# Optimization experiments

Hardware: AMD Instinct MI355X
Metric: run time of the kernel (lower is better)

The kernel has to match this reference:

```python
import jax, jax.numpy as jnp
import numpy as np

NUM_SEGMENTS = 64
HIDDEN = 1024
RANK = 16
N = 8192


def _xavier(key, shape):
    fan_in, fan_out = shape[-2], shape[-1]
    limit = (6.0 / (fan_in + fan_out)) ** 0.5
    return jax.random.uniform(key, shape, jnp.float32, -limit, limit)


def setup_inputs() -> dict:
    key = jax.random.key(0)
    k1, k2, k3, k4 = jax.random.split(key, 4)
    return {
        "math_hidden_states": jax.random.normal(k1, (N, HIDDEN), jnp.float32),
        "segment_ids": jax.random.randint(k2, (N,), 0, NUM_SEGMENTS, jnp.int64),
        "A_matrices": _xavier(k3, (NUM_SEGMENTS, HIDDEN, RANK)),
        "B_matrices": _xavier(k4, (NUM_SEGMENTS, RANK, HIDDEN)),
        "bias": jnp.zeros((NUM_SEGMENTS, HIDDEN), jnp.float32),
    }


def reference(math_hidden_states, segment_ids, A_matrices, B_matrices, bias):
    # gather per-token low-rank factors: A [N,H,R], B [N,R,H]
    gathered_A = A_matrices[segment_ids]
    gathered_B = B_matrices[segment_ids]
    # intermediate = B @ x  -> [N, R]
    intermediate = jnp.einsum('nrh,nh->nr', gathered_B, math_hidden_states)
    # transformed = A @ intermediate -> [N, H]
    transformed = jnp.einsum('nhr,nr->nh', gathered_A, intermediate)
    return transformed + bias[segment_ids]
```

## Files before the change

kernel.cpp:

```cpp
#include <hip/hip_runtime.h>

#define HID 1024
#define RANK 16
#define NSEG 64
#define G 16
#define NXCD 8


__global__ __launch_bounds__(1024) void k_hist_scan(
    const int* __restrict__ seg, int N,
    int* __restrict__ base_g, int* __restrict__ cursor_g,
    int* __restrict__ desc_g, int gtiles)
{
    __shared__ int hist[NSEG];
    __shared__ int ltot;
    const int tid = threadIdx.x;
    if (tid < NSEG) hist[tid] = 0;
    __syncthreads();
    for (int i = tid; i < N; i += 1024) atomicAdd(&hist[seg[i]], 1);
    __syncthreads();

    if (tid < 64) {
        const int h = hist[tid];
        const int p = (h + 15) & ~15;
        int v = p;
        #pragma unroll
        for (int off = 1; off < 64; off <<= 1) {
            int u = __shfl_up(v, off, 64);
            if (tid >= off) v += u;
        }
        const int b = v - p;
        base_g[tid]   = b;
        cursor_g[tid] = 0;
        if (tid == 63) ltot = v;
        const int nt = (h + 15) >> 4;
        for (int k = 0; k < nt; ++k) {
            const int cnt = min(16, h - (k << 4));
            desc_g[(b >> 4) + k] = (tid << 19) | (cnt << 14) | (b + (k << 4));
        }
    }
    __syncthreads();
    const int totTiles = ltot >> 4;
    for (int t = totTiles + tid; t < gtiles; t += 1024) desc_g[t] = -1;
}

__global__ __launch_bounds__(256) void k_scatter(
    const int* __restrict__ seg, int N,
    const int* __restrict__ base_g, int* __restrict__ cursor_g,
    int* __restrict__ sorted)
{
    const int i = blockIdx.x * 256 + threadIdx.x;
    if (i < N) {
        const int s = seg[i];
        const int pos = atomicAdd(&cursor_g[s], 1);
        sorted[base_g[s] + pos] = i;
    }
}

__global__ __launch_bounds__(256) void k_apply(
    const float* __restrict__ x,
    const int*   __restrict__ sorted,
    const int*   __restrict__ desc,
    const float* __restrict__ A,
    const float* __restrict__ B,
    const float* __restrict__ bias,
    float*       __restrict__ out,
    int chunkPerXcd)
{
    const int work = (blockIdx.x & (NXCD - 1)) * chunkPerXcd + (blockIdx.x >> 3);
    const int d = desc[work];
    if (d < 0) return;
    const int s     = d >> 19;
    const int cnt   = (d >> 14) & 31;
    const int start = d & 16383;

    const int tid  = threadIdx.x;
    const int lane = tid & 63;
    const int w    = tid >> 6;

    __shared__ float4 x_lds[G][HID / 4];
    __shared__ float  red[4][16][68];
    __shared__ float  inter_lds[G][RANK];

    const int n0 = sorted[start];

    #pragma unroll
    for (int jj = 0; jj < 4; ++jj) {
        const int j  = w * 4 + jj;
        const int nj = (j < cnt) ? sorted[start + j] : n0;
        const float4* xr = (const float4*)(x + (size_t)nj * HID);
        #pragma unroll
        for (int k = 0; k < 4; ++k)
            x_lds[j][k * 64 + lane] = xr[k * 64 + lane];
    }

    int n[G];
    #pragma unroll
    for (int j = 0; j < G; ++j)
        n[j] = (j < cnt) ? sorted[start + j] : n0;

    __syncthreads();

    const float4* B4 = (const float4*)(B + (size_t)s * RANK * HID);
    float acc[4][G];
    #pragma unroll
    for (int rr = 0; rr < 4; ++rr)
        #pragma unroll
        for (int j = 0; j < G; ++j) acc[rr][j] = 0.f;

    #pragma unroll
    for (int k = 0; k < 4; ++k) {
        float4 b[4];
        #pragma unroll
        for (int rr = 0; rr < 4; ++rr)
            b[rr] = B4[(size_t)(w * 4 + rr) * (HID / 4) + k * 64 + lane];
        #pragma unroll
        for (int j = 0; j < G; ++j) {
            const float4 xj = x_lds[j][k * 64 + lane];
            #pragma unroll
            for (int rr = 0; rr < 4; ++rr)
                acc[rr][j] += b[rr].x * xj.x + b[rr].y * xj.y
                            + b[rr].z * xj.z + b[rr].w * xj.w;
        }
    }

    const int v = lane & 15;
    const int q = lane >> 4;
    #pragma unroll
    for (int p = 0; p < 4; ++p) {
        #pragma unroll
        for (int idx = 0; idx < 16; ++idx)
            red[w][idx][lane] = acc[idx >> 2][p * 4 + (idx & 3)];
        const float4* rp = (const float4*)&red[w][v][q * 16];
        float4 r0 = rp[0], r1 = rp[1], r2 = rp[2], r3 = rp[3];
        float sum = ((r0.x + r0.y) + (r0.z + r0.w))
                  + ((r1.x + r1.y) + (r1.z + r1.w))
                  + ((r2.x + r2.y) + (r2.z + r2.w))
                  + ((r3.x + r3.y) + (r3.z + r3.w));
        sum += __shfl_xor(sum, 16, 64);
        sum += __shfl_xor(sum, 32, 64);
        if (lane < 16)
            inter_lds[p * 4 + (v & 3)][w * 4 + (v >> 2)] = sum;
    }
    __syncthreads();

    const float4* A4 = (const float4*)(A + (size_t)s * HID * RANK);
    float4 av[4][4];
    #pragma unroll
    for (int jh = 0; jh < 4; ++jh)
        #pragma unroll
        for (int qq = 0; qq < 4; ++qq)
            av[jh][qq] = A4[(size_t)(tid * 4 + jh) * (RANK / 4) + qq];
    const float4 bia = ((const float4*)(bias + (size_t)s * HID))[tid];

    #pragma unroll
    for (int j = 0; j < G; ++j) {
        const float4* I4 = (const float4*)inter_lds[j];
        float4 iv[4];
        #pragma unroll
        for (int qq = 0; qq < 4; ++qq) iv[qq] = I4[qq];
        float4 o = bia;
        float* op = (float*)&o;
        #pragma unroll
        for (int jh = 0; jh < 4; ++jh) {
            float a = 0.f;
            #pragma unroll
            for (int qq = 0; qq < 4; ++qq)
                a += av[jh][qq].x * iv[qq].x + av[jh][qq].y * iv[qq].y
                   + av[jh][qq].z * iv[qq].z + av[jh][qq].w * iv[qq].w;
            op[jh] += a;
        }
        if (j < cnt)
            ((float4*)(out + (size_t)n[j] * HID))[tid] = o;
    }
}

extern "C" void kernel_launch(void* const* d_in, const int* in_sizes, int n_in,
                              void* d_out, int out_size, void* d_ws, size_t ws_size,
                              hipStream_t stream) {
    const float* x    = (const float*)d_in[0];
    const int*   seg  = (const int*)d_in[1];
    const float* A    = (const float*)d_in[2];
    const float* B    = (const float*)d_in[3];
    const float* bias = (const float*)d_in[4];
    float* out = (float*)d_out;

    const int N = in_sizes[1];
    const int gtiles = (((N + G - 1) / G) + NSEG + 7) & ~7;

    int* wsi    = (int*)d_ws;
    int* base_g = wsi;
    int* cursor = wsi + NSEG;
    int* desc   = wsi + 2 * NSEG;
    int* sorted = wsi + 2 * NSEG + gtiles;

    k_hist_scan<<<1, 1024, 0, stream>>>(seg, N, base_g, cursor, desc, gtiles);
    k_scatter  <<<(N + 255) / 256, 256, 0, stream>>>(seg, N, base_g, cursor, sorted);
    k_apply    <<<gtiles, 256, 0, stream>>>(x, sorted, desc, A, B, bias, out,
                                            gtiles / NXCD);
}
```

Measured before the change: 143.0 us.

## Split fused low-rank apply into split-K intermediate and output kernels

The single fused gather/B-projection/A-projection kernel is replaced by two kernels. Tiles grow to 32 tokens per segment. The first kernel splits the hidden dimension into 4 chunks, keeps the B slice in registers, and writes partial rank-16 intermediates to workspace. The second kernel reduces the 4 partials and computes a 256-wide slice of the output per block. This targets more parallelism and no LDS staging of x, at the cost of an extra launch, a global round trip for the partials, and more padding per segment.

```diff
diff --git a/kernel.cpp b/kernel.cpp
--- a/kernel.cpp
+++ b/kernel.cpp
@@ -3,7 +3,8 @@
 #define HID 1024
 #define RANK 16
 #define NSEG 64
-#define G 16
+#define T 32
+#define KC 4
 #define NXCD 8
 
 
@@ -22,7 +23,7 @@
 
     if (tid < 64) {
         const int h = hist[tid];
-        const int p = (h + 15) & ~15;
+        const int p = (h + T - 1) & ~(T - 1);
         int v = p;
         #pragma unroll
         for (int off = 1; off < 64; off <<= 1) {
@@ -33,15 +34,14 @@
         base_g[tid]   = b;
         cursor_g[tid] = 0;
         if (tid == 63) ltot = v;
-        const int nt = (h + 15) >> 4;
+        const int nt = (h + T - 1) >> 5;
         for (int k = 0; k < nt; ++k) {
-            const int cnt = min(16, h - (k << 4));
-            desc_g[(b >> 4) + k] = (tid << 19) | (cnt << 14) | (b + (k << 4));
+            const int cnt = min(T, h - (k << 5));
+            desc_g[(b >> 5) + k] = (tid << 20) | (cnt << 14) | (b + (k << 5));
         }
     }
     __syncthreads();
-    const int totTiles = ltot >> 4;
-    for (int t = totTiles + tid; t < gtiles; t += 1024) desc_g[t] = -1;
+    for (int t = (ltot >> 5) + tid; t < gtiles; t += 1024) desc_g[t] = -1;
 }
 
 __global__ __launch_bounds__(256) void k_scatter(
@@ -57,80 +57,54 @@
     }
 }
 
-__global__ __launch_bounds__(256) void k_apply(
+__global__ __launch_bounds__(256) void k_inter(
     const float* __restrict__ x,
     const int*   __restrict__ sorted,
     const int*   __restrict__ desc,
-    const float* __restrict__ A,
     const float* __restrict__ B,
-    const float* __restrict__ bias,
-    float*       __restrict__ out,
+    float*       __restrict__ part,
     int chunkPerXcd)
 {
-    const int work = (blockIdx.x & (NXCD - 1)) * chunkPerXcd + (blockIdx.x >> 3);
-    const int d = desc[work];
+    const int bid  = blockIdx.x;
+    const int work = (bid & (NXCD - 1)) * chunkPerXcd + (bid >> 3);
+    const int tile = work >> 2;
+    const int c    = work & 3;
+    const int d = desc[tile];
     if (d < 0) return;
-    const int s     = d >> 19;
-    const int cnt   = (d >> 14) & 31;
+    const int s     = d >> 20;
+    const int cnt   = (d >> 14) & 63;
     const int start = d & 16383;
 
     const int tid  = threadIdx.x;
     const int lane = tid & 63;
     const int w    = tid >> 6;
 
-    __shared__ float4 x_lds[G][HID / 4];
-    __shared__ float  red[4][16][68];
-    __shared__ float  inter_lds[G][RANK];
+    __shared__ float red[4][16][68];
+
+    const float4* B4 = (const float4*)B + (size_t)s * (RANK * HID / 4);
+    float4 br[16];
+    #pragma unroll
+    for (int r = 0; r < 16; ++r)
+        br[r] = B4[r * (HID / 4) + c * 64 + lane];
 
     const int n0 = sorted[start];
+    const int v  = lane & 15;
+    const int q  = lane >> 4;
+    float* outp = part + ((size_t)tile * KC + c) * (T * RANK);
 
     #pragma unroll
-    for (int jj = 0; jj < 4; ++jj) {
-        const int j  = w * 4 + jj;
-        const int nj = (j < cnt) ? sorted[start + j] : n0;
-        const float4* xr = (const float4*)(x + (size_t)nj * HID);
+    for (int j = 0; j < 8; ++j) {
+        const int tok = w * 8 + j;
+        const int nj  = (tok < cnt) ? sorted[start + tok] : n0;
+        const float4 xv = ((const float4*)x)[(size_t)nj * (HID / 4) + c * 64 + lane];
+
+        float acc[16];
         #pragma unroll
-        for (int k = 0; k < 4; ++k)
-            x_lds[j][k * 64 + lane] = xr[k * 64 + lane];
-    }
-
-    int n[G];
-    #pragma unroll
-    for (int j = 0; j < G; ++j)
-        n[j] = (j < cnt) ? sorted[start + j] : n0;
-
-    __syncthreads();
-
-    const float4* B4 = (const float4*)(B + (size_t)s * RANK * HID);
-    float acc[4][G];
-    #pragma unroll
-    for (int rr = 0; rr < 4; ++rr)
+        for (int r = 0; r < 16; ++r)
+            acc[r] = br[r].x * xv.x + br[r].y * xv.y + br[r].z * xv.z + br[r].w * xv.w;
+
         #pragma unroll
-        for (int j = 0; j < G; ++j) acc[rr][j] = 0.f;
-
-    #pragma unroll
-    for (int k = 0; k < 4; ++k) {
-        float4 b[4];
-        #pragma unroll
-        for (int rr = 0; rr < 4; ++rr)
-            b[rr] = B4[(size_t)(w * 4 + rr) * (HID / 4) + k * 64 + lane];
-        #pragma unroll
-        for (int j = 0; j < G; ++j) {
-            const float4 xj = x_lds[j][k * 64 + lane];
-            #pragma unroll
-            for (int rr = 0; rr < 4; ++rr)
-                acc[rr][j] += b[rr].x * xj.x + b[rr].y * xj.y
-                            + b[rr].z * xj.z + b[rr].w * xj.w;
-        }
-    }
-
-    const int v = lane & 15;
-    const int q = lane >> 4;
-    #pragma unroll
-    for (int p = 0; p < 4; ++p) {
-        #pragma unroll
-        for (int idx = 0; idx < 16; ++idx)
-            red[w][idx][lane] = acc[idx >> 2][p * 4 + (idx & 3)];
+        for (int r = 0; r < 16; ++r) red[w][r][lane] = acc[r];
         const float4* rp = (const float4*)&red[w][v][q * 16];
         float4 r0 = rp[0], r1 = rp[1], r2 = rp[2], r3 = rp[3];
         float sum = ((r0.x + r0.y) + (r0.z + r0.w))
@@ -139,39 +113,65 @@
                   + ((r3.x + r3.y) + (r3.z + r3.w));
         sum += __shfl_xor(sum, 16, 64);
         sum += __shfl_xor(sum, 32, 64);
-        if (lane < 16)
-            inter_lds[p * 4 + (v & 3)][w * 4 + (v >> 2)] = sum;
-    }
-    __syncthreads();
-
-    const float4* A4 = (const float4*)(A + (size_t)s * HID * RANK);
-    float4 av[4][4];
+        if (lane < 16) outp[tok * RANK + v] = sum;
+    }
+}
+
+__global__ __launch_bounds__(256) void k_out(
+    const int*   __restrict__ sorted,
+    const int*   __restrict__ desc,
+    const float* __restrict__ A,
+    const float* __restrict__ bias,
+    const float* __restrict__ part,
+    float*       __restrict__ out,
+    int chunkPerXcd)
+{
+    const int bid  = blockIdx.x;
+    const int work = (bid & (NXCD - 1)) * chunkPerXcd + (bid >> 3);
+    const int tile = work >> 2;
+    const int hc   = work & 3;
+    const int d = desc[tile];
+    if (d < 0) return;
+    const int s     = d >> 20;
+    const int cnt   = (d >> 14) & 63;
+    const int start = d & 16383;
+
+    const int tid = threadIdx.x;
+
+    __shared__ float2 inter2[T * RANK / 2];
+    __shared__ int    tok_lds[T];
+
+    if (tid < T) tok_lds[tid] = (tid < cnt) ? sorted[start + tid] : -1;
+
+    {
+        const float2* p2 = (const float2*)(part + (size_t)tile * KC * (T * RANK));
+        float2 a0 = p2[tid], a1 = p2[256 + tid], a2 = p2[512 + tid], a3 = p2[768 + tid];
+        inter2[tid] = make_float2(a0.x + a1.x + a2.x + a3.x,
+                                  a0.y + a1.y + a2.y + a3.y);
+    }
+
+    const float4* A4 = (const float4*)A + (size_t)s * (HID * RANK / 4);
+    float4 av[4];
     #pragma unroll
-    for (int jh = 0; jh < 4; ++jh)
-        #pragma unroll
-        for (int qq = 0; qq < 4; ++qq)
-            av[jh][qq] = A4[(size_t)(tid * 4 + jh) * (RANK / 4) + qq];
-    const float4 bia = ((const float4*)(bias + (size_t)s * HID))[tid];
-
-    #pragma unroll
-    for (int j = 0; j < G; ++j) {
-        const float4* I4 = (const float4*)inter_lds[j];
-        float4 iv[4];
-        #pragma unroll
-        for (int qq = 0; qq < 4; ++qq) iv[qq] = I4[qq];
-        float4 o = bia;
-        float* op = (float*)&o;
-        #pragma unroll
-        for (int jh = 0; jh < 4; ++jh) {
-            float a = 0.f;
-            #pragma unroll
-            for (int qq = 0; qq < 4; ++qq)
-                a += av[jh][qq].x * iv[qq].x + av[jh][qq].y * iv[qq].y
-                   + av[jh][qq].z * iv[qq].z + av[jh][qq].w * iv[qq].w;
-            op[jh] += a;
-        }
-        if (j < cnt)
-            ((float4*)(out + (size_t)n[j] * HID))[tid] = o;
+    for (int qq = 0; qq < 4; ++qq)
+        av[qq] = A4[(size_t)(hc * 256 + tid) * (RANK / 4) + qq];
+    const float bi = bias[(size_t)s * HID + hc * 256 + tid];
+
+    __syncthreads();
+
+    const float* il = (const float*)inter2;
+    #pragma unroll 8
+    for (int j = 0; j < T; ++j) {
+        const int nj = tok_lds[j];
+        const float4* iv = (const float4*)&il[j * RANK];
+        float4 i0 = iv[0], i1 = iv[1], i2 = iv[2], i3 = iv[3];
+        float o = bi
+            + av[0].x * i0.x + av[0].y * i0.y + av[0].z * i0.z + av[0].w * i0.w
+            + av[1].x * i1.x + av[1].y * i1.y + av[1].z * i1.z + av[1].w * i1.w
+            + av[2].x * i2.x + av[2].y * i2.y + av[2].z * i2.z + av[2].w * i2.w
+            + av[3].x * i3.x + av[3].y * i3.y + av[3].z * i3.z + av[3].w * i3.w;
+        if (nj >= 0)
+            out[(size_t)nj * HID + hc * 256 + tid] = o;
     }
 }
 
@@ -186,16 +186,18 @@
     float* out = (float*)d_out;
 
     const int N = in_sizes[1];
-    const int gtiles = (((N + G - 1) / G) + NSEG + 7) & ~7;
+    const int gtiles = (((N + T - 1) / T) + NSEG + 7) & ~7;
 
     int* wsi    = (int*)d_ws;
     int* base_g = wsi;
     int* cursor = wsi + NSEG;
     int* desc   = wsi + 2 * NSEG;
     int* sorted = wsi + 2 * NSEG + gtiles;
-
+    float* part = (float*)(wsi + 2 * NSEG + gtiles + gtiles * T);
+
+    const int grid = gtiles * 4;
     k_hist_scan<<<1, 1024, 0, stream>>>(seg, N, base_g, cursor, desc, gtiles);
     k_scatter  <<<(N + 255) / 256, 256, 0, stream>>>(seg, N, base_g, cursor, sorted);
-    k_apply    <<<gtiles, 256, 0, stream>>>(x, sorted, desc, A, B, bias, out,
-                                            gtiles / NXCD);
-}
+    k_inter    <<<grid, 256, 0, stream>>>(x, sorted, desc, B, part, grid / NXCD);
+    k_out      <<<grid, 256, 0, stream>>>(sorted, desc, A, bias, part, out, grid / NXCD);
+}
```

Measured after the change: 131.1 us. 1.09x faster.
